# Kernel tuning notes

Measured on AMD Instinct MI355X. Metric: run time of the kernel, lower is better.

The kernel has to match this reference:

```python
import jax, jax.numpy as jnp
import numpy as np

EPS = 1e-5

def bn(x, gamma, beta, axes):
    # training-mode batchnorm over `axes`, channel axis = 1 (matches nn.BatchNorm1d/2d)
    mean = jnp.mean(x, axis=axes, keepdims=True)
    var = jnp.var(x, axis=axes, keepdims=True)
    shp = [1] * x.ndim
    shp[1] = -1
    return gamma.reshape(shp) * (x - mean) * jax.lax.rsqrt(var + EPS) + beta.reshape(shp)

def setup_inputs():
    key = jax.random.key(0)
    B, N, K, Cin, Cout, m = 4, 4096, 32, 64, 64, 8
    ks = jax.random.split(key, 10)
    def w(k, shape, fan_in):
        return jax.random.normal(k, shape, jnp.float32) * np.float32(np.sqrt(2.0 / fan_in))
    return {
        "x": jax.random.normal(ks[0], (B, Cin, N), jnp.float32),
        "xyz_score": jax.random.normal(ks[1], (B, 66, N, K), jnp.float32),
        "conv1_w": w(ks[2], (Cin, Cin), Cin),
        "bn1_g": jnp.ones((Cin,), jnp.float32), "bn1_b": jnp.zeros((Cin,), jnp.float32),
        "matrice2": w(ks[3], (Cin, m * Cout), Cin),  # weight bank: i x (m*o)
        "sn_w0": w(ks[4], (64, 66), 66), "sn_g0": jnp.ones((64,), jnp.float32), "sn_b0": jnp.zeros((64,), jnp.float32),
        "sn_w1": w(ks[5], (32, 64), 64), "sn_g1": jnp.ones((32,), jnp.float32), "sn_b1": jnp.zeros((32,), jnp.float32),
        "sn_w2": w(ks[6], (16, 32), 32), "sn_g2": jnp.ones((16,), jnp.float32), "sn_b2": jnp.zeros((16,), jnp.float32),
        "sn_w3": w(ks[7], (m, 16), 16), "sn_bias3": jnp.zeros((m,), jnp.float32),
        "bn2_g": jnp.ones((Cout,), jnp.float32), "bn2_b": jnp.zeros((Cout,), jnp.float32),
        "idx": jax.random.randint(ks[8], (B, N, K), 0, N, dtype=jnp.int32),
    }

def reference(x, xyz_score, conv1_w, bn1_g, bn1_b, matrice2,
              sn_w0, sn_g0, sn_b0, sn_w1, sn_g1, sn_b1, sn_w2, sn_g2, sn_b2,
              sn_w3, sn_bias3, bn2_g, bn2_b, idx):
    B, Cin, N = x.shape
    m = sn_w3.shape[0]
    # conv1 (1x1, no bias) + BN1 + ReLU  -> [B, Cin, N]
    h = jnp.einsum('oc,bcn->bon', conv1_w, x)
    h = jax.nn.relu(bn(h, bn1_g, bn1_b, (0, 2)))
    # feat_trans_pointnet: [B,N,Cin] @ [Cin, m*Cout] -> [B,N,m,Cout]
    y = jnp.einsum('bcn,ck->bnk', h, matrice2).reshape(B, N, m, -1)
    # ScoreNet: stack of 1x1 conv2d + BN + ReLU, final conv with bias, softmax over m
    s = xyz_score  # [B, 66, N, K]
    s = jax.nn.relu(bn(jnp.einsum('oc,bcnk->bonk', sn_w0, s), sn_g0, sn_b0, (0, 2, 3)))
    s = jax.nn.relu(bn(jnp.einsum('oc,bcnk->bonk', sn_w1, s), sn_g1, sn_b1, (0, 2, 3)))
    s = jax.nn.relu(bn(jnp.einsum('oc,bcnk->bonk', sn_w2, s), sn_g2, sn_b2, (0, 2, 3)))
    s = jnp.einsum('oc,bcnk->bonk', sn_w3, s) + sn_bias3[None, :, None, None]
    score = jax.nn.softmax(s, axis=1)            # [B, m, N, K], bias=0
    score = jnp.transpose(score, (0, 2, 3, 1))   # [B, N, K, m]
    # assemble_pointnet: gather neighbor transformed feats and score-weight them
    neigh = y[jnp.arange(B)[:, None, None], idx]             # [B, N, K, m, Cout]
    out = jnp.einsum('bnkm,bnkmo->bon', score, neigh)        # [B, Cout, N]
    return jax.nn.relu(bn(out, bn2_g, bn2_b, (0, 2)))
```

## Files before the change

kernel.cpp:

```cpp
#include <hip/hip_runtime.h>
#include <cstdint>

typedef unsigned short u16;
typedef unsigned int   u32;
typedef __attribute__((ext_vector_type(8))) short short8;
typedef __attribute__((ext_vector_type(4))) float f32x4;

constexpr int CB = 4;
constexpr int CN = 4096;
constexpr int CK = 32;
constexpr int NPTS = CB * CN * CK;
constexpr int NBK  = 131072;
constexpr float EPSV = 1e-5f;

struct __align__(16) Q4 { u32 a, b, c, d; };

static __device__ __forceinline__ u16 f2b(float f) {
  union { float f; u32 u; } v; v.f = f;
  u32 u = v.u;
  return (u16)((u + 0x7FFFu + ((u >> 16) & 1u)) >> 16);
}
static __device__ __forceinline__ float b2f(u16 h) {
  union { u32 u; float f; } v; v.u = ((u32)h) << 16;
  return v.f;
}
static __device__ __forceinline__ u32 pk2(float lo, float hi) {
  return (u32)f2b(lo) | ((u32)f2b(hi) << 16);
}
static __device__ __forceinline__ short8 mk8(u32 a, u32 b, u32 c, u32 d) {
  union { u32 w[4]; short8 v; } u; u.w[0]=a; u.w[1]=b; u.w[2]=c; u.w[3]=d; return u.v;
}

__global__ __launch_bounds__(256) void k_conv1(const float* __restrict__ x,
                                               const float* __restrict__ w,
                                               float* __restrict__ h,
                                               float* S, float* Q) {
  __shared__ float wl[16 * 64];
  __shared__ float ls[32];
  int tid = threadIdx.x;
  int og = blockIdx.x >> 6;
  int cb = blockIdx.x & 63;
  for (int i = tid; i < 1024; i += 256) wl[i] = w[og * 1024 + i];
  if (tid < 32) ls[tid] = 0.f;
  __syncthreads();
  int col = cb * 256 + tid;
  int b = col >> 12, n = col & 4095;
  float xr[64];
  const float* xp = x + (size_t)(b * 64) * CN + n;
  #pragma unroll
  for (int c = 0; c < 64; ++c) xr[c] = xp[(size_t)c * CN];
  int lane = tid & 63;
  for (int oo = 0; oo < 16; ++oo) {
    int o = og * 16 + oo;
    float acc = 0.f;
    const float* wr = &wl[oo * 64];
    #pragma unroll
    for (int c = 0; c < 64; ++c) acc = fmaf(wr[c], xr[c], acc);
    h[(size_t)(b * 64 + o) * CN + n] = acc;
    float v = acc, v2 = acc * acc;
    for (int d = 1; d < 64; d <<= 1) { v += __shfl_xor(v, d); v2 += __shfl_xor(v2, d); }
    if (lane == 0) { atomicAdd(&ls[oo], v); atomicAdd(&ls[16 + oo], v2); }
  }
  __syncthreads();
  if (tid < 16) atomicAdd(&S[og * 16 + tid], ls[tid]);
  else if (tid < 32) atomicAdd(&Q[og * 16 + tid - 16], ls[tid]);
}

__global__ __launch_bounds__(64) void k_affine(const float* S, const float* Q,
                                               const float* g, const float* bt,
                                               float* A, float* Bo, int C, float inv_cnt) {
  int t = threadIdx.x;
  if (t < C) {
    float mean = S[t] * inv_cnt;
    float var = fmaxf(Q[t] * inv_cnt - mean * mean, 0.f);
    float a = g[t] * rsqrtf(var + EPSV);
    A[t] = a;
    Bo[t] = bt[t] - mean * a;
  }
}

__global__ __launch_bounds__(256) void k_prepM2(const float* __restrict__ M2,
                                                u16* __restrict__ m2frag) {
  int i = blockIdx.x * 256 + threadIdx.x;
  int e = i & 7, lane = (i >> 3) & 63, t = i >> 9;
  int mt = t >> 1, kc = t & 1;
  int row = 16 * mt + (lane & 15);
  int k = 32 * kc + 8 * (lane >> 4) + e;
  m2frag[i] = f2b(M2[k * 512 + row]);
}

__global__ __launch_bounds__(256) void k_y(const float* __restrict__ h,
                                           const u16* __restrict__ m2frag,
                                           const float* __restrict__ Ah,
                                           const float* __restrict__ Bh,
                                           u16* __restrict__ y16) {
  __shared__ u16 yl[4][16 * 520];
  __shared__ float abl[128];
  int tid = threadIdx.x;
  if (tid < 64) abl[tid] = Ah[tid];
  else if (tid < 128) abl[tid] = Bh[tid - 64];
  int wv = tid >> 6, lane = tid & 63, g = lane >> 4, pl = lane & 15;
  __syncthreads();
  int wid = blockIdx.x * 4 + wv;
  int n0 = wid * 16;
  int b = n0 >> 12, nloc = n0 & 4095;
  const float* sb = h + (size_t)(b * 64) * CN + nloc + pl;
  u32 w[8];
  #pragma unroll
  for (int kc = 0; kc < 2; ++kc) {
    #pragma unroll
    for (int e2 = 0; e2 < 4; ++e2) {
      int c0 = 32 * kc + 8 * g + 2 * e2;
      float v0 = fmaxf(fmaf(abl[c0],     sb[(size_t)c0 * CN],       abl[64 + c0]),     0.f);
      float v1 = fmaxf(fmaf(abl[c0 + 1], sb[(size_t)(c0 + 1) * CN], abl[64 + c0 + 1]), 0.f);
      w[kc * 4 + e2] = pk2(v0, v1);
    }
  }
  short8 Bf0 = mk8(w[0], w[1], w[2], w[3]);
  short8 Bf1 = mk8(w[4], w[5], w[6], w[7]);
  const short8* m2f = (const short8*)m2frag;
  u16* ylw = &yl[wv][0];
  #pragma unroll
  for (int mt = 0; mt < 32; ++mt) {
    short8 A0 = m2f[(mt * 2 + 0) * 64 + lane];
    short8 A1 = m2f[(mt * 2 + 1) * 64 + lane];
    f32x4 z = {0.f, 0.f, 0.f, 0.f};
    z = __builtin_amdgcn_mfma_f32_16x16x32_bf16(A0, Bf0, z, 0, 0, 0);
    z = __builtin_amdgcn_mfma_f32_16x16x32_bf16(A1, Bf1, z, 0, 0, 0);
    u32* wp = (u32*)&ylw[pl * 520 + 16 * mt + 4 * g];
    wp[0] = pk2(z[0], z[1]);
    wp[1] = pk2(z[2], z[3]);
  }
  u16* yg = y16 + (size_t)n0 * 512;
  for (int j = 0; j < 16; ++j) {
    short8 v = *(const short8*)&yl[wv][j * 520 + lane * 8];
    *(short8*)(yg + (size_t)j * 512 + lane * 8) = v;
  }
}

static __device__ __forceinline__ void ld_frags(const float* __restrict__ xyz,
                                                int c, int g, int pl, short8 fr[5]) {
  int pbase = c * 32;
  int b = pbase >> 17, r = pbase & (NBK - 1);
  const float* base = xyz + (size_t)b * 66 * NBK + r + g * 8;
  #pragma unroll
  for (int ci = 0; ci < 4; ++ci) {
    const float* p = base + (size_t)(16 * ci + pl) * NBK;
    float4 v0 = *(const float4*)p;
    float4 v1 = *(const float4*)(p + 4);
    fr[ci] = mk8(pk2(v0.x, v0.y), pk2(v0.z, v0.w), pk2(v1.x, v1.y), pk2(v1.z, v1.w));
  }
  if (pl < 2) {
    const float* p = base + (size_t)(64 + pl) * NBK;
    float4 v0 = *(const float4*)p;
    float4 v1 = *(const float4*)(p + 4);
    fr[4] = mk8(pk2(v0.x, v0.y), pk2(v0.z, v0.w), pk2(v1.x, v1.y), pk2(v1.z, v1.w));
  } else if (pl == 2) {
    fr[4] = mk8(0x3F803F80u, 0x3F803F80u, 0x3F803F80u, 0x3F803F80u);
  } else {
    fr[4] = mk8(0u, 0u, 0u, 0u);
  }
}

__global__ __launch_bounds__(256) void k_moment(const float* __restrict__ xyz,
                                                float* __restrict__ Mpart) {
  constexpr int TI[15] = {0,0,0,0,0,1,1,1,1,2,2,2,3,3,4};
  constexpr int TJ[15] = {0,1,2,3,4,1,2,3,4,2,3,4,3,4,4};
  int tid = threadIdx.x;
  int wv = tid >> 6;
  int wid = blockIdx.x * 4 + wv;
  int lane = tid & 63, g = lane >> 4, pl = lane & 15;
  f32x4 acc[15];
  #pragma unroll
  for (int t = 0; t < 15; ++t) acc[t] = (f32x4){0.f, 0.f, 0.f, 0.f};
  for (int cc = wid; cc < NPTS / 32; cc += 4096) {
    short8 fr0[5], fr1[5];
    ld_frags(xyz, cc,        g, pl, fr0);
    ld_frags(xyz, cc + 2048, g, pl, fr1);
    #pragma unroll
    for (int t = 0; t < 15; ++t)
      acc[t] = __builtin_amdgcn_mfma_f32_16x16x32_bf16(fr0[TI[t]], fr0[TJ[t]], acc[t], 0, 0, 0);
    #pragma unroll
    for (int t = 0; t < 15; ++t)
      acc[t] = __builtin_amdgcn_mfma_f32_16x16x32_bf16(fr1[TI[t]], fr1[TJ[t]], acc[t], 0, 0, 0);
  }
  float* mp = Mpart + (size_t)wid * 3840;
  #pragma unroll
  for (int t = 0; t < 15; ++t)
    *(f32x4*)(mp + t * 256 + lane * 4) = acc[t];
}

__global__ __launch_bounds__(256) void k_mreduce(const float* __restrict__ Mpart,
                                                 float* __restrict__ M) {
  int e = blockIdx.x * 256 + threadIdx.x;
  int kg = blockIdx.y;
  float s = 0.f;
  for (int k = kg * 256; k < kg * 256 + 256; ++k) s += Mpart[(size_t)k * 3840 + e];
  atomicAdd(&M[e], s);
}

__global__ __launch_bounds__(256) void k_affine1m(const float* __restrict__ M,
                                                  const float* __restrict__ w0,
                                                  const float* __restrict__ g0,
                                                  const float* __restrict__ b0,
                                                  float* __restrict__ A1,
                                                  float* __restrict__ B1) {
  __shared__ float lsM[67 * 68];
  __shared__ float w0l[64 * 69];
  __shared__ float red[4 * 64];
  int tid = threadIdx.x;
  const float inv = 1.f / (float)NPTS;
  for (int i = tid; i < 67 * 67; i += 256) {
    int r = i / 67, c = i % 67;
    int rr = r, cc = c;
    if ((r >> 4) > (c >> 4)) { rr = c; cc = r; }
    int ti = rr >> 4, tj = cc >> 4;
    int t = ti * (9 - ti) / 2 + tj;
    int rho = rr & 15, kap = cc & 15;
    lsM[r * 68 + c] = M[t * 256 + ((rho >> 2) * 16 + kap) * 4 + (rho & 3)] * inv;
  }
  for (int i = tid; i < 64 * 66; i += 256) {
    int o = i / 66, c = i % 66;
    w0l[o * 69 + c] = w0[i];
  }
  __syncthreads();
  int o = tid & 63, sl = tid >> 6;
  float acc2 = 0.f;
  for (int c1 = sl * 17; c1 < sl * 17 + 17; ++c1) {
    if (c1 >= 66) break;
    float inner = 0.f;
    const float* mr = &lsM[c1 * 68];
    const float* wr = &w0l[o * 69];
    for (int c2 = 0; c2 < 66; ++c2) inner = fmaf(mr[c2], wr[c2], inner);
    acc2 = fmaf(wr[c1], inner, acc2);
  }
  red[sl * 64 + o] = acc2;
  __syncthreads();
  if (sl == 0) {
    float Ez2 = red[o] + red[64 + o] + red[128 + o] + red[192 + o];
    float mean = 0.f;
    const float* wr = &w0l[o * 69];
    for (int c = 0; c < 66; ++c) mean = fmaf(wr[c], lsM[c * 68 + 66], mean);
    float var = fmaxf(Ez2 - mean * mean, 0.f);
    float a = g0[o] * rsqrtf(var + EPSV);
    A1[o] = a;
    B1[o] = b0[o] - mean * a;
  }
}

__global__ __launch_bounds__(256) void k_prep(const float* __restrict__ w0,
                                              const float* __restrict__ w1,
                                              const float* __restrict__ A1,
                                              const float* __restrict__ B1,
                                              u16* __restrict__ w0frag,
                                              u16* __restrict__ w1frag) {
  int tid = threadIdx.x;
  for (int i = tid; i < 6144; i += 256) {
    int e = i & 7, lane = (i >> 3) & 63, t = i >> 9;
    int mt = t / 3, kc = t % 3;
    int row = 16 * mt + (lane & 15);
    int k = 32 * kc + 8 * (lane >> 4) + e;
    float v;
    if (k < 66)      v = A1[row] * w0[row * 66 + k];
    else if (k == 66) v = B1[row];
    else              v = 0.f;
    w0frag[i] = f2b(v);
  }
  for (int i = tid; i < 2048; i += 256) {
    int e = i & 7, lane = (i >> 3) & 63, t = i >> 9;
    int m2t = t >> 1, kc2 = t & 1;
    int row = 16 * m2t + (lane & 15);
    int k = 32 * kc2 + 8 * (lane >> 4) + e;
    w1frag[i] = f2b(w1[row * 64 + k]);
  }
}

__global__ __launch_bounds__(256) void k_s2(const float* __restrict__ xyz,
                                            const u16* __restrict__ w0frag,
                                            const u16* __restrict__ w1frag,
                                            u32* __restrict__ z2p,
                                            float* S, float* Q) {
  __shared__ u16 a1l[4][16][88];
  __shared__ float ls2[64];
  int tid = threadIdx.x;
  int wv = tid >> 6, lane = tid & 63, g = lane >> 4, pl = lane & 15;
  if (tid < 64) ls2[tid] = 0.f;
  __syncthreads();

  const short8* w0f = (const short8*)w0frag;
  const short8* w1f = (const short8*)w1frag;
  short8 A0[4][3];
  #pragma unroll
  for (int mt = 0; mt < 4; ++mt)
    #pragma unroll
    for (int kc = 0; kc < 3; ++kc) A0[mt][kc] = w0f[(mt * 3 + kc) * 64 + lane];
  short8 W1f[2][2];
  #pragma unroll
  for (int m2t = 0; m2t < 2; ++m2t)
    #pragma unroll
    for (int kc2 = 0; kc2 < 2; ++kc2) W1f[m2t][kc2] = w1f[(m2t * 2 + kc2) * 64 + lane];

  float sum8[8], sq8[8];
  #pragma unroll
  for (int i = 0; i < 8; ++i) { sum8[i] = 0.f; sq8[i] = 0.f; }

  int wid = blockIdx.x * 4 + wv;
  for (int s = wid; s < NPTS / 32; s += 8192) {
    int pgA = s * 16;
    int pgB = pgA + 262144;
    int bA = pgA >> 17, rA = pgA & (NBK - 1);
    int bB = pgB >> 17, rB = pgB & (NBK - 1);
    const float* sbA = xyz + (size_t)bA * 66 * NBK + rA + pl;
    const float* sbB = xyz + (size_t)bB * 66 * NBK + rB + pl;
    float vA[16], vB[16];
    #pragma unroll
    for (int e = 0; e < 8; ++e) vA[e]     = sbA[(size_t)(8 * g + e) * NBK];
    #pragma unroll
    for (int e = 0; e < 8; ++e) vA[8 + e] = sbA[(size_t)(32 + 8 * g + e) * NBK];
    #pragma unroll
    for (int e = 0; e < 8; ++e) vB[e]     = sbB[(size_t)(8 * g + e) * NBK];
    #pragma unroll
    for (int e = 0; e < 8; ++e) vB[8 + e] = sbB[(size_t)(32 + 8 * g + e) * NBK];
    float v64A = 0.f, v65A = 0.f, v64B = 0.f, v65B = 0.f;
    if (g == 0) {
      v64A = sbA[(size_t)64 * NBK]; v65A = sbA[(size_t)65 * NBK];
      v64B = sbB[(size_t)64 * NBK]; v65B = sbB[(size_t)65 * NBK];
    }
    {
      u32 c2a = 0u, c2b = 0u;
      if (g == 0) { c2a = pk2(v64A, v65A); c2b = 0x00003F80u; }
      short8 Bf0 = mk8(pk2(vA[0], vA[1]), pk2(vA[2], vA[3]), pk2(vA[4], vA[5]), pk2(vA[6], vA[7]));
      short8 Bf1 = mk8(pk2(vA[8], vA[9]), pk2(vA[10], vA[11]), pk2(vA[12], vA[13]), pk2(vA[14], vA[15]));
      short8 Bf2 = mk8(c2a, c2b, 0u, 0u);
      #pragma unroll
      for (int mt = 0; mt < 4; ++mt) {
        f32x4 z = {0.f, 0.f, 0.f, 0.f};
        z = __builtin_amdgcn_mfma_f32_16x16x32_bf16(A0[mt][0], Bf0, z, 0, 0, 0);
        z = __builtin_amdgcn_mfma_f32_16x16x32_bf16(A0[mt][1], Bf1, z, 0, 0, 0);
        z = __builtin_amdgcn_mfma_f32_16x16x32_bf16(A0[mt][2], Bf2, z, 0, 0, 0);
        float r0 = fmaxf(z[0], 0.f), r1 = fmaxf(z[1], 0.f);
        float r2 = fmaxf(z[2], 0.f), r3 = fmaxf(z[3], 0.f);
        u32* wp = (u32*)&a1l[wv][pl][16 * mt + 4 * g];
        wp[0] = pk2(r0, r1);
        wp[1] = pk2(r2, r3);
      }
      short8 B2f0 = *(const short8*)&a1l[wv][pl][8 * g];
      short8 B2f1 = *(const short8*)&a1l[wv][pl][32 + 8 * g];
      #pragma unroll
      for (int m2t = 0; m2t < 2; ++m2t) {
        f32x4 z2 = {0.f, 0.f, 0.f, 0.f};
        z2 = __builtin_amdgcn_mfma_f32_16x16x32_bf16(W1f[m2t][0], B2f0, z2, 0, 0, 0);
        z2 = __builtin_amdgcn_mfma_f32_16x16x32_bf16(W1f[m2t][1], B2f1, z2, 0, 0, 0);
        #pragma unroll
        for (int rr = 0; rr < 4; ++rr) {
          sum8[m2t * 4 + rr] += z2[rr];
          sq8[m2t * 4 + rr] += z2[rr] * z2[rr];
        }
        int jlo = 8 * m2t + 2 * g;
        z2p[(size_t)jlo * NPTS + pgA + pl]       = pk2(z2[0], z2[1]);
        z2p[(size_t)(jlo + 1) * NPTS + pgA + pl] = pk2(z2[2], z2[3]);
      }
    }
    {
      u32 c2a = 0u, c2b = 0u;
      if (g == 0) { c2a = pk2(v64B, v65B); c2b = 0x00003F80u; }
      short8 Bf0 = mk8(pk2(vB[0], vB[1]), pk2(vB[2], vB[3]), pk2(vB[4], vB[5]), pk2(vB[6], vB[7]));
      short8 Bf1 = mk8(pk2(vB[8], vB[9]), pk2(vB[10], vB[11]), pk2(vB[12], vB[13]), pk2(vB[14], vB[15]));
      short8 Bf2 = mk8(c2a, c2b, 0u, 0u);
      #pragma unroll
      for (int mt = 0; mt < 4; ++mt) {
        f32x4 z = {0.f, 0.f, 0.f, 0.f};
        z = __builtin_amdgcn_mfma_f32_16x16x32_bf16(A0[mt][0], Bf0, z, 0, 0, 0);
        z = __builtin_amdgcn_mfma_f32_16x16x32_bf16(A0[mt][1], Bf1, z, 0, 0, 0);
        z = __builtin_amdgcn_mfma_f32_16x16x32_bf16(A0[mt][2], Bf2, z, 0, 0, 0);
        float r0 = fmaxf(z[0], 0.f), r1 = fmaxf(z[1], 0.f);
        float r2 = fmaxf(z[2], 0.f), r3 = fmaxf(z[3], 0.f);
        u32* wp = (u32*)&a1l[wv][pl][16 * mt + 4 * g];
        wp[0] = pk2(r0, r1);
        wp[1] = pk2(r2, r3);
      }
      short8 B2f0 = *(const short8*)&a1l[wv][pl][8 * g];
      short8 B2f1 = *(const short8*)&a1l[wv][pl][32 + 8 * g];
      #pragma unroll
      for (int m2t = 0; m2t < 2; ++m2t) {
        f32x4 z2 = {0.f, 0.f, 0.f, 0.f};
        z2 = __builtin_amdgcn_mfma_f32_16x16x32_bf16(W1f[m2t][0], B2f0, z2, 0, 0, 0);
        z2 = __builtin_amdgcn_mfma_f32_16x16x32_bf16(W1f[m2t][1], B2f1, z2, 0, 0, 0);
        #pragma unroll
        for (int rr = 0; rr < 4; ++rr) {
          sum8[m2t * 4 + rr] += z2[rr];
          sq8[m2t * 4 + rr] += z2[rr] * z2[rr];
        }
        int jlo = 8 * m2t + 2 * g;
        z2p[(size_t)jlo * NPTS + pgB + pl]       = pk2(z2[0], z2[1]);
        z2p[(size_t)(jlo + 1) * NPTS + pgB + pl] = pk2(z2[2], z2[3]);
      }
    }
  }
  #pragma unroll
  for (int i = 0; i < 8; ++i) {
    float vS = sum8[i], vQ = sq8[i];
    for (int d = 1; d < 16; d <<= 1) { vS += __shfl_xor(vS, d); vQ += __shfl_xor(vQ, d); }
    if (pl == 0) {
      int ch = 16 * (i >> 2) + 4 * g + (i & 3);
      atomicAdd(&ls2[ch], vS);
      atomicAdd(&ls2[32 + ch], vQ);
    }
  }
  __syncthreads();
  if (tid < 32) atomicAdd(&S[tid], ls2[tid]);
  else if (tid < 64) atomicAdd(&Q[tid - 32], ls2[tid]);
}

__global__ __launch_bounds__(256) void k_s3(const u32* __restrict__ z2p,
                                            const float* __restrict__ w2,
                                            const float* __restrict__ A2,
                                            const float* __restrict__ B2,
                                            u32* __restrict__ z3,
                                            float* S, float* Q) {
  __shared__ float w2l[16 * 32];
  __shared__ float ab[64];
  __shared__ float ls[32];
  int tid = threadIdx.x;
  for (int i = tid; i < 512; i += 256) w2l[i] = w2[i];
  if (tid < 32) { ab[tid] = A2[tid]; ls[tid] = 0.f; }
  else if (tid < 64) ab[tid] = B2[tid - 32];
  __syncthreads();
  int p = blockIdx.x * 256 + tid;
  float a2[32];
  #pragma unroll
  for (int j = 0; j < 16; ++j) {
    u32 wj = z2p[(size_t)j * NPTS + p];
    float lo = b2f((u16)(wj & 0xFFFFu));
    float hi = b2f((u16)(wj >> 16));
    a2[2 * j]     = fmaxf(fmaf(ab[2 * j], lo, ab[32 + 2 * j]), 0.f);
    a2[2 * j + 1] = fmaxf(fmaf(ab[2 * j + 1], hi, ab[32 + 2 * j + 1]), 0.f);
  }
  int lane = tid & 63;
  float zt[16];
  for (int j = 0; j < 16; ++j) {
    float z = 0.f;
    const float* wr = &w2l[j * 32];
    #pragma unroll
    for (int c = 0; c < 32; ++c) z = fmaf(wr[c], a2[c], z);
    zt[j] = z;
    float v = z, v2 = z * z;
    for (int d = 1; d < 64; d <<= 1) { v += __shfl_xor(v, d); v2 += __shfl_xor(v2, d); }
    if (lane == 0) { atomicAdd(&ls[j], v); atomicAdd(&ls[16 + j], v2); }
  }
  u32 pkk[8];
  #pragma unroll
  for (int j = 0; j < 8; ++j) pkk[j] = pk2(zt[2 * j], zt[2 * j + 1]);
  Q4* dst = (Q4*)(z3 + (size_t)p * 8);
  #pragma unroll
  for (int i = 0; i < 2; ++i) { Q4 q; q.a = pkk[4*i]; q.b = pkk[4*i+1]; q.c = pkk[4*i+2]; q.d = pkk[4*i+3]; dst[i] = q; }
  __syncthreads();
  if (tid < 16) atomicAdd(&S[tid], ls[tid]);
  else if (tid < 32) atomicAdd(&Q[tid - 16], ls[tid]);
}

__global__ __launch_bounds__(256) void k_score(const u32* __restrict__ z3,
                                               const float* __restrict__ w3,
                                               const float* __restrict__ bias3,
                                               const float* __restrict__ A3,
                                               const float* __restrict__ B3,
                                               float* __restrict__ scores) {
  __shared__ float w3l[128];
  __shared__ float bl[8];
  __shared__ float ab[32];
  int tid = threadIdx.x;
  if (tid < 128) w3l[tid] = w3[tid];
  if (tid < 8) bl[tid] = bias3[tid];
  if (tid < 16) ab[tid] = A3[tid];
  else if (tid < 32) ab[tid] = B3[tid - 16];
  __syncthreads();
  int p = blockIdx.x * 256 + tid;
  const Q4* zp = (const Q4*)(z3 + (size_t)p * 8);
  Q4 r0 = zp[0], r1 = zp[1];
  u32 w8[8] = {r0.a, r0.b, r0.c, r0.d, r1.a, r1.b, r1.c, r1.d};
  float a3[16];
  #pragma unroll
  for (int t = 0; t < 8; ++t) {
    int c = t * 2;
    a3[c]     = fmaxf(fmaf(ab[c], b2f((u16)(w8[t] & 0xFFFFu)), ab[16 + c]), 0.f);
    a3[c + 1] = fmaxf(fmaf(ab[c + 1], b2f((u16)(w8[t] >> 16)), ab[16 + c + 1]), 0.f);
  }
  float z4[8]; float mx = -1e30f;
  #pragma unroll
  for (int mI = 0; mI < 8; ++mI) {
    float z = bl[mI];
    const float* wr = &w3l[mI * 16];
    #pragma unroll
    for (int c = 0; c < 16; ++c) z = fmaf(wr[c], a3[c], z);
    z4[mI] = z; mx = fmaxf(mx, z);
  }
  float ssum = 0.f;
  #pragma unroll
  for (int mI = 0; mI < 8; ++mI) { z4[mI] = __expf(z4[mI] - mx); ssum += z4[mI]; }
  float inv = 1.f / ssum;
  float4* sp = (float4*)(scores + (size_t)p * 8);
  sp[0] = make_float4(z4[0] * inv, z4[1] * inv, z4[2] * inv, z4[3] * inv);
  sp[1] = make_float4(z4[4] * inv, z4[5] * inv, z4[6] * inv, z4[7] * inv);
}

__global__ __launch_bounds__(256) void k_gather(const u16* __restrict__ y16,
                                                const float* __restrict__ scores,
                                                const int* __restrict__ idx,
                                                float* __restrict__ out0,
                                                float* S, float* Q) {
  __shared__ float ls[128];
  int tid = threadIdx.x;
  if (tid < 128) ls[tid] = 0.f;
  __syncthreads();
  int bid = blockIdx.x;
  int batch = (bid & 7) >> 1;
  int sub = ((bid >> 3) << 1) | (bid & 1);
  int wv = tid >> 6, lane = tid & 63;
  int m = lane >> 3, og = lane & 7;
  const u16* ybase = y16 + (size_t)batch * CN * 512;
  int pid0 = (batch << 12) + sub * 8 + wv * 2;
  int pbase = pid0 * 32;
  int jv = idx[pbase + lane];
  float acc0[8] = {0, 0, 0, 0, 0, 0, 0, 0};
  float acc1[8] = {0, 0, 0, 0, 0, 0, 0, 0};
  #pragma unroll 4
  for (int k = 0; k < 32; ++k) {
    int j0 = __shfl(jv, k);
    int j1 = __shfl(jv, 32 + k);
    float s0 = scores[(size_t)(pbase + k) * 8 + m];
    float s1 = scores[(size_t)(pbase + 32 + k) * 8 + m];
    short8 y0 = *(const short8*)(ybase + ((size_t)j0 << 9) + lane * 8);
    short8 y1 = *(const short8*)(ybase + ((size_t)j1 << 9) + lane * 8);
    #pragma unroll
    for (int t = 0; t < 8; ++t) {
      acc0[t] = fmaf(s0, b2f((u16)y0[t]), acc0[t]);
      acc1[t] = fmaf(s1, b2f((u16)y1[t]), acc1[t]);
    }
  }
  #pragma unroll
  for (int d = 8; d < 64; d <<= 1) {
    #pragma unroll
    for (int t = 0; t < 8; ++t) {
      acc0[t] += __shfl_xor(acc0[t], d);
      acc1[t] += __shfl_xor(acc1[t], d);
    }
  }
  if (m == 0) {
    float* op0 = out0 + (size_t)pid0 * 64 + og * 8;
    *(float4*)op0       = make_float4(acc0[0], acc0[1], acc0[2], acc0[3]);
    *(float4*)(op0 + 4) = make_float4(acc0[4], acc0[5], acc0[6], acc0[7]);
    float* op1 = out0 + (size_t)(pid0 + 1) * 64 + og * 8;
    *(float4*)op1       = make_float4(acc1[0], acc1[1], acc1[2], acc1[3]);
    *(float4*)(op1 + 4) = make_float4(acc1[4], acc1[5], acc1[6], acc1[7]);
    #pragma unroll
    for (int t = 0; t < 8; ++t) {
      float sv = acc0[t] + acc1[t];
      float qv = acc0[t] * acc0[t] + acc1[t] * acc1[t];
      atomicAdd(&ls[og * 8 + t], sv);
      atomicAdd(&ls[64 + og * 8 + t], qv);
    }
  }
  __syncthreads();
  if (tid < 64) atomicAdd(&S[tid], ls[tid]);
  else if (tid < 128) atomicAdd(&Q[tid - 64], ls[tid]);
}

__global__ __launch_bounds__(256) void k_bn2(const float* __restrict__ out0,
                                             const float* __restrict__ A,
                                             const float* __restrict__ Bo,
                                             float* __restrict__ outp) {
  int gid = blockIdx.x * 256 + threadIdx.x;
  for (int i = gid; i < CB * 64 * CN; i += 262144) {
    int b = i >> 18, o = (i >> 12) & 63, n = i & 4095;
    float v = out0[((size_t)((b << 12) | n)) * 64 + o];
    outp[i] = fmaxf(fmaf(A[o], v, Bo[o]), 0.f);
  }
}

extern "C" void kernel_launch(void* const* d_in, const int* in_sizes, int n_in,
                              void* d_out, int out_size, void* d_ws, size_t ws_size,
                              hipStream_t stream) {
  const float* x       = (const float*)d_in[0];
  const float* xyz     = (const float*)d_in[1];
  const float* conv1_w = (const float*)d_in[2];
  const float* bn1_g   = (const float*)d_in[3];
  const float* bn1_b   = (const float*)d_in[4];
  const float* M2      = (const float*)d_in[5];
  const float* w0      = (const float*)d_in[6];
  const float* g0      = (const float*)d_in[7];
  const float* b0      = (const float*)d_in[8];
  const float* w1      = (const float*)d_in[9];
  const float* g1      = (const float*)d_in[10];
  const float* b1      = (const float*)d_in[11];
  const float* w2      = (const float*)d_in[12];
  const float* g2      = (const float*)d_in[13];
  const float* b2      = (const float*)d_in[14];
  const float* w3      = (const float*)d_in[15];
  const float* bias3   = (const float*)d_in[16];
  const float* bn2_g   = (const float*)d_in[17];
  const float* bn2_b   = (const float*)d_in[18];
  const int*   idx     = (const int*)d_in[19];
  float* out = (float*)d_out;

  char* wsb = (char*)d_ws;
  float* h      = (float*)wsb;
  u16*   y16    = (u16*)(wsb + 4194304);
  float* scores = (float*)(wsb + 20971520);
  u32*   z2p    = (u32*)(wsb + 37748736);
  u32*   z3     = (u32*)(wsb + 71303168);
  float* out0   = (float*)(wsb + 88080384);
  float* sums   = (float*)(wsb + 92274688);
  float* S_h = sums;        float* Q_h = sums + 64;
  float* S_2 = sums + 128;  float* Q_2 = sums + 160;
  float* S_3 = sums + 192;  float* Q_3 = sums + 208;
  float* S_o = sums + 224;  float* Q_o = sums + 288;
  float* Mm  = sums + 352;
  float* A_h = sums + 6752; float* B_h = sums + 6816;
  float* A_1 = sums + 6880; float* B_1 = sums + 6944;
  float* A_2 = sums + 7008; float* B_2 = sums + 7040;
  float* A_3 = sums + 7072; float* B_3 = sums + 7088;
  float* A_o = sums + 7104; float* B_o = sums + 7168;
  u16* w0frag = (u16*)(sums + 7232);
  u16* w1frag = w0frag + 6144;
  u16* m2frag = w1frag + 2048;
  float* Mpart = (float*)z2p;

  hipMemsetAsync(sums, 0, 6752 * sizeof(float), stream);

  k_prepM2<<<128, 256, 0, stream>>>(M2, m2frag);
  k_conv1<<<256, 256, 0, stream>>>(x, conv1_w, h, S_h, Q_h);
  k_affine<<<1, 64, 0, stream>>>(S_h, Q_h, bn1_g, bn1_b, A_h, B_h, 64, 1.f / 16384.f);
  k_y<<<256, 256, 0, stream>>>(h, m2frag, A_h, B_h, y16);

  k_moment<<<512, 256, 0, stream>>>(xyz, Mpart);
  k_mreduce<<<dim3(15, 8), 256, 0, stream>>>(Mpart, Mm);
  k_affine1m<<<1, 256, 0, stream>>>(Mm, w0, g0, b0, A_1, B_1);
  k_prep<<<1, 256, 0, stream>>>(w0, w1, A_1, B_1, w0frag, w1frag);
  k_s2<<<2048, 256, 0, stream>>>(xyz, w0frag, w1frag, z2p, S_2, Q_2);
  k_affine<<<1, 64, 0, stream>>>(S_2, Q_2, g1, b1, A_2, B_2, 32, 1.f / (float)NPTS);
  k_s3<<<2048, 256, 0, stream>>>(z2p, w2, A_2, B_2, z3, S_3, Q_3);
  k_affine<<<1, 64, 0, stream>>>(S_3, Q_3, g2, b2, A_3, B_3, 16, 1.f / (float)NPTS);

  k_score<<<2048, 256, 0, stream>>>(z3, w3, bias3, A_3, B_3, scores);
  k_gather<<<2048, 256, 0, stream>>>(y16, scores, idx, out0, S_o, Q_o);
  k_affine<<<1, 64, 0, stream>>>(S_o, Q_o, bn2_g, bn2_b, A_o, B_o, 64, 1.f / 16384.f);
  k_bn2<<<1024, 256, 0, stream>>>(out0, A_o, B_o, out);
}
```

Baseline: 311.2 us.

## Fuse moment pass with bf16 point-major transpose of xyz_score for ScoreNet layer

The moment kernel now stages each 1024-point chunk of xyz_score through shared memory as bf16 and, besides accumulating the second-moment matrix, writes a point-major bf16 copy (80 channels per point, padded, with a ones channel). The second ScoreNet kernel then reads 16-byte fragments from this compact copy instead of re-reading the fp32 channel-strided input with scalar loads. This targets the second full fp32 read of the 138 MB input. It costs an extra ~84 MB write and read of the bf16 copy, plus LDS use that may lower occupancy. The launch is also moved earlier in the stream.

```diff
diff --git a/kernel.cpp b/kernel.cpp
--- a/kernel.cpp
+++ b/kernel.cpp
@@ -138,52 +138,67 @@
   }
 }
 
-static __device__ __forceinline__ void ld_frags(const float* __restrict__ xyz,
-                                                int c, int g, int pl, short8 fr[5]) {
-  int pbase = c * 32;
-  int b = pbase >> 17, r = pbase & (NBK - 1);
-  const float* base = xyz + (size_t)b * 66 * NBK + r + g * 8;
-  #pragma unroll
-  for (int ci = 0; ci < 4; ++ci) {
-    const float* p = base + (size_t)(16 * ci + pl) * NBK;
-    float4 v0 = *(const float4*)p;
-    float4 v1 = *(const float4*)(p + 4);
-    fr[ci] = mk8(pk2(v0.x, v0.y), pk2(v0.z, v0.w), pk2(v1.x, v1.y), pk2(v1.z, v1.w));
-  }
-  if (pl < 2) {
-    const float* p = base + (size_t)(64 + pl) * NBK;
-    float4 v0 = *(const float4*)p;
-    float4 v1 = *(const float4*)(p + 4);
-    fr[4] = mk8(pk2(v0.x, v0.y), pk2(v0.z, v0.w), pk2(v1.x, v1.y), pk2(v1.z, v1.w));
-  } else if (pl == 2) {
-    fr[4] = mk8(0x3F803F80u, 0x3F803F80u, 0x3F803F80u, 0x3F803F80u);
-  } else {
-    fr[4] = mk8(0u, 0u, 0u, 0u);
-  }
-}
-
-__global__ __launch_bounds__(256) void k_moment(const float* __restrict__ xyz,
-                                                float* __restrict__ Mpart) {
+__global__ __launch_bounds__(256) void k_transmom(const float* __restrict__ xyz,
+                                                  float* __restrict__ Mpart,
+                                                  u16* __restrict__ xyz16t) {
   constexpr int TI[15] = {0,0,0,0,0,1,1,1,1,2,2,2,3,3,4};
   constexpr int TJ[15] = {0,1,2,3,4,1,2,3,4,2,3,4,3,4,4};
-  int tid = threadIdx.x;
-  int wv = tid >> 6;
-  int wid = blockIdx.x * 4 + wv;
-  int lane = tid & 63, g = lane >> 4, pl = lane & 15;
+  __shared__ u16 tile[66 * 264];
+  int tid = threadIdx.x;
+  int bid = blockIdx.x;
+  int wv = tid >> 6, lane = tid & 63, g = lane >> 4, pl = lane & 15;
+  int b = bid >> 7;
+  int rbase = (bid & 127) * 1024;
+  const float* xb = xyz + (size_t)b * 66 * NBK;
   f32x4 acc[15];
   #pragma unroll
   for (int t = 0; t < 15; ++t) acc[t] = (f32x4){0.f, 0.f, 0.f, 0.f};
-  for (int cc = wid; cc < NPTS / 32; cc += 4096) {
-    short8 fr0[5], fr1[5];
-    ld_frags(xyz, cc,        g, pl, fr0);
-    ld_frags(xyz, cc + 2048, g, pl, fr1);
-    #pragma unroll
-    for (int t = 0; t < 15; ++t)
-      acc[t] = __builtin_amdgcn_mfma_f32_16x16x32_bf16(fr0[TI[t]], fr0[TJ[t]], acc[t], 0, 0, 0);
-    #pragma unroll
-    for (int t = 0; t < 15; ++t)
-      acc[t] = __builtin_amdgcn_mfma_f32_16x16x32_bf16(fr1[TI[t]], fr1[TJ[t]], acc[t], 0, 0, 0);
-  }
+  const short8 ones8 = mk8(0x3F803F80u, 0x3F803F80u, 0x3F803F80u, 0x3F803F80u);
+  const short8 zero8 = mk8(0u, 0u, 0u, 0u);
+
+  for (int ck = 0; ck < 4; ++ck) {
+    int r = rbase + ck * 256;
+    for (int s = tid; s < 4224; s += 256) {
+      int c = s >> 6, f4 = s & 63;
+      float4 v = *(const float4*)(xb + (size_t)c * NBK + r + f4 * 4);
+      u32* wp = (u32*)&tile[c * 264 + f4 * 4];
+      wp[0] = pk2(v.x, v.y);
+      wp[1] = pk2(v.z, v.w);
+    }
+    __syncthreads();
+    #pragma unroll
+    for (int grp = 0; grp < 2; ++grp) {
+      int pt0 = wv * 64 + grp * 32;
+      short8 fr[5];
+      #pragma unroll
+      for (int ci = 0; ci < 4; ++ci)
+        fr[ci] = *(const short8*)&tile[(16 * ci + pl) * 264 + pt0 + 8 * g];
+      if (pl < 2)       fr[4] = *(const short8*)&tile[(64 + pl) * 264 + pt0 + 8 * g];
+      else if (pl == 2) fr[4] = ones8;
+      else              fr[4] = zero8;
+      #pragma unroll
+      for (int t = 0; t < 15; ++t)
+        acc[t] = __builtin_amdgcn_mfma_f32_16x16x32_bf16(fr[TI[t]], fr[TJ[t]], acc[t], 0, 0, 0);
+    }
+    {
+      int gpt = bid * 1024 + ck * 256 + tid;
+      u16* dst = xyz16t + (size_t)gpt * 80;
+      #pragma unroll
+      for (int i = 0; i < 10; ++i) {
+        u32 wd[4];
+        #pragma unroll
+        for (int j = 0; j < 4; ++j) {
+          int c0 = 8 * i + 2 * j;
+          u32 lo = (c0 < 66)     ? (u32)tile[c0 * 264 + tid]       : (c0 == 66 ? 0x3F80u : 0u);
+          u32 hi = (c0 + 1 < 66) ? (u32)tile[(c0 + 1) * 264 + tid] : (c0 + 1 == 66 ? 0x3F80u : 0u);
+          wd[j] = lo | (hi << 16);
+        }
+        *(short8*)(dst + i * 8) = mk8(wd[0], wd[1], wd[2], wd[3]);
+      }
+    }
+    __syncthreads();
+  }
+  int wid = bid * 4 + wv;
   float* mp = Mpart + (size_t)wid * 3840;
   #pragma unroll
   for (int t = 0; t < 15; ++t)
@@ -275,7 +290,7 @@
   }
 }
 
-__global__ __launch_bounds__(256) void k_s2(const float* __restrict__ xyz,
+__global__ __launch_bounds__(256) void k_s2(const u16* __restrict__ xyz16t,
                                             const u16* __restrict__ w0frag,
                                             const u16* __restrict__ w1frag,
                                             u32* __restrict__ z2p,
@@ -303,41 +318,27 @@
   float sum8[8], sq8[8];
   #pragma unroll
   for (int i = 0; i < 8; ++i) { sum8[i] = 0.f; sq8[i] = 0.f; }
+  const short8 zero8 = mk8(0u, 0u, 0u, 0u);
 
   int wid = blockIdx.x * 4 + wv;
   for (int s = wid; s < NPTS / 32; s += 8192) {
     int pgA = s * 16;
     int pgB = pgA + 262144;
-    int bA = pgA >> 17, rA = pgA & (NBK - 1);
-    int bB = pgB >> 17, rB = pgB & (NBK - 1);
-    const float* sbA = xyz + (size_t)bA * 66 * NBK + rA + pl;
-    const float* sbB = xyz + (size_t)bB * 66 * NBK + rB + pl;
-    float vA[16], vB[16];
-    #pragma unroll
-    for (int e = 0; e < 8; ++e) vA[e]     = sbA[(size_t)(8 * g + e) * NBK];
-    #pragma unroll
-    for (int e = 0; e < 8; ++e) vA[8 + e] = sbA[(size_t)(32 + 8 * g + e) * NBK];
-    #pragma unroll
-    for (int e = 0; e < 8; ++e) vB[e]     = sbB[(size_t)(8 * g + e) * NBK];
-    #pragma unroll
-    for (int e = 0; e < 8; ++e) vB[8 + e] = sbB[(size_t)(32 + 8 * g + e) * NBK];
-    float v64A = 0.f, v65A = 0.f, v64B = 0.f, v65B = 0.f;
-    if (g == 0) {
-      v64A = sbA[(size_t)64 * NBK]; v65A = sbA[(size_t)65 * NBK];
-      v64B = sbB[(size_t)64 * NBK]; v65B = sbB[(size_t)65 * NBK];
-    }
+    const u16* tpA = xyz16t + (size_t)(pgA + pl) * 80;
+    const u16* tpB = xyz16t + (size_t)(pgB + pl) * 80;
+    short8 BfA0 = *(const short8*)(tpA + 8 * g);
+    short8 BfA1 = *(const short8*)(tpA + 32 + 8 * g);
+    short8 BfA2 = (g < 2) ? *(const short8*)(tpA + 64 + 8 * g) : zero8;
+    short8 BfB0 = *(const short8*)(tpB + 8 * g);
+    short8 BfB1 = *(const short8*)(tpB + 32 + 8 * g);
+    short8 BfB2 = (g < 2) ? *(const short8*)(tpB + 64 + 8 * g) : zero8;
     {
-      u32 c2a = 0u, c2b = 0u;
-      if (g == 0) { c2a = pk2(v64A, v65A); c2b = 0x00003F80u; }
-      short8 Bf0 = mk8(pk2(vA[0], vA[1]), pk2(vA[2], vA[3]), pk2(vA[4], vA[5]), pk2(vA[6], vA[7]));
-      short8 Bf1 = mk8(pk2(vA[8], vA[9]), pk2(vA[10], vA[11]), pk2(vA[12], vA[13]), pk2(vA[14], vA[15]));
-      short8 Bf2 = mk8(c2a, c2b, 0u, 0u);
       #pragma unroll
       for (int mt = 0; mt < 4; ++mt) {
         f32x4 z = {0.f, 0.f, 0.f, 0.f};
-        z = __builtin_amdgcn_mfma_f32_16x16x32_bf16(A0[mt][0], Bf0, z, 0, 0, 0);
-        z = __builtin_amdgcn_mfma_f32_16x16x32_bf16(A0[mt][1], Bf1, z, 0, 0, 0);
-        z = __builtin_amdgcn_mfma_f32_16x16x32_bf16(A0[mt][2], Bf2, z, 0, 0, 0);
+        z = __builtin_amdgcn_mfma_f32_16x16x32_bf16(A0[mt][0], BfA0, z, 0, 0, 0);
+        z = __builtin_amdgcn_mfma_f32_16x16x32_bf16(A0[mt][1], BfA1, z, 0, 0, 0);
+        z = __builtin_amdgcn_mfma_f32_16x16x32_bf16(A0[mt][2], BfA2, z, 0, 0, 0);
         float r0 = fmaxf(z[0], 0.f), r1 = fmaxf(z[1], 0.f);
         float r2 = fmaxf(z[2], 0.f), r3 = fmaxf(z[3], 0.f);
         u32* wp = (u32*)&a1l[wv][pl][16 * mt + 4 * g];
@@ -362,17 +363,12 @@
       }
     }
     {
-      u32 c2a = 0u, c2b = 0u;
-      if (g == 0) { c2a = pk2(v64B, v65B); c2b = 0x00003F80u; }
-      short8 Bf0 = mk8(pk2(vB[0], vB[1]), pk2(vB[2], vB[3]), pk2(vB[4], vB[5]), pk2(vB[6], vB[7]));
-      short8 Bf1 = mk8(pk2(vB[8], vB[9]), pk2(vB[10], vB[11]), pk2(vB[12], vB[13]), pk2(vB[14], vB[15]));
-      short8 Bf2 = mk8(c2a, c2b, 0u, 0u);
       #pragma unroll
       for (int mt = 0; mt < 4; ++mt) {
         f32x4 z = {0.f, 0.f, 0.f, 0.f};
-        z = __builtin_amdgcn_mfma_f32_16x16x32_bf16(A0[mt][0], Bf0, z, 0, 0, 0);
-        z = __builtin_amdgcn_mfma_f32_16x16x32_bf16(A0[mt][1], Bf1, z, 0, 0, 0);
-        z = __builtin_amdgcn_mfma_f32_16x16x32_bf16(A0[mt][2], Bf2, z, 0, 0, 0);
+        z = __builtin_amdgcn_mfma_f32_16x16x32_bf16(A0[mt][0], BfB0, z, 0, 0, 0);
+        z = __builtin_amdgcn_mfma_f32_16x16x32_bf16(A0[mt][1], BfB1, z, 0, 0, 0);
+        z = __builtin_amdgcn_mfma_f32_16x16x32_bf16(A0[mt][2], BfB2, z, 0, 0, 0);
         float r0 = fmaxf(z[0], 0.f), r1 = fmaxf(z[1], 0.f);
         float r2 = fmaxf(z[2], 0.f), r3 = fmaxf(z[3], 0.f);
         u32* wp = (u32*)&a1l[wv][pl][16 * mt + 4 * g];
@@ -610,6 +606,7 @@
   u32*   z3     = (u32*)(wsb + 71303168);
   float* out0   = (float*)(wsb + 88080384);
   float* sums   = (float*)(wsb + 92274688);
+  u16*   xyz16t = (u16*)(wsb + 100663296);
   float* S_h = sums;        float* Q_h = sums + 64;
   float* S_2 = sums + 128;  float* Q_2 = sums + 160;
   float* S_3 = sums + 192;  float* Q_3 = sums + 208;
@@ -628,15 +625,15 @@
   hipMemsetAsync(sums, 0, 6752 * sizeof(float), stream);
 
   k_prepM2<<<128, 256, 0, stream>>>(M2, m2frag);
+  k_transmom<<<512, 256, 0, stream>>>(xyz, Mpart, xyz16t);
   k_conv1<<<256, 256, 0, stream>>>(x, conv1_w, h, S_h, Q_h);
   k_affine<<<1, 64, 0, stream>>>(S_h, Q_h, bn1_g, bn1_b, A_h, B_h, 64, 1.f / 16384.f);
   k_y<<<256, 256, 0, stream>>>(h, m2frag, A_h, B_h, y16);
 
-  k_moment<<<512, 256, 0, stream>>>(xyz, Mpart);
   k_mreduce<<<dim3(15, 8), 256, 0, stream>>>(Mpart, Mm);
   k_affine1m<<<1, 256, 0, stream>>>(Mm, w0, g0, b0, A_1, B_1);
   k_prep<<<1, 256, 0, stream>>>(w0, w1, A_1, B_1, w0frag, w1frag);
-  k_s2<<<2048, 256, 0, stream>>>(xyz, w0frag, w1frag, z2p, S_2, Q_2);
+  k_s2<<<2048, 256, 0, stream>>>(xyz16t, w0frag, w1frag, z2p, S_2, Q_2);
   k_affine<<<1, 64, 0, stream>>>(S_2, Q_2, g1, b1, A_2, B_2, 32, 1.f / (float)NPTS);
   k_s3<<<2048, 256, 0, stream>>>(z2p, w2, A_2, B_2, z3, S_3, Q_3);
   k_affine<<<1, 64, 0, stream>>>(S_3, Q_3, g2, b2, A_3, B_3, 16, 1.f / (float)NPTS);
```

New measurement: 343.0 us. +10.2%, slower.
